# Performance work log

Measured on AMD Instinct MI355X. Metric: run time of the kernel, lower is better.

The kernel has to match this reference:

```python
import jax, jax.numpy as jnp
import numpy as np

N_NODES = 50000
N_EDGES = 640000
IN_FEATS = 512
HID = 128
OUT_FEATS = 128
N_GRAPHS = 256


def setup_inputs() -> dict:
    key = jax.random.key(0)
    ks = jax.random.split(key, 7)
    x = jax.random.normal(ks[0], (N_NODES, IN_FEATS), dtype=jnp.float32)
    edge_index = jax.random.randint(ks[1], (2, N_EDGES), 0, N_NODES, dtype=jnp.int32)
    batch = jnp.sort(jax.random.randint(ks[2], (N_NODES,), 0, N_GRAPHS, dtype=jnp.int32))
    W1 = jax.random.normal(ks[3], (IN_FEATS, HID), dtype=jnp.float32) * (1.0 / np.sqrt(IN_FEATS))
    b1 = jnp.zeros((HID,), jnp.float32)
    W2 = jax.random.normal(ks[4], (HID, OUT_FEATS), dtype=jnp.float32) * (1.0 / np.sqrt(HID))
    b2 = jnp.zeros((OUT_FEATS,), jnp.float32)
    return {"x": x, "W1": W1, "b1": b1, "W2": W2, "b2": b2,
            "edge_index": edge_index, "batch": batch}


def reference(x, W1, b1, W2, b2, edge_index, batch):
    N = x.shape[0]
    loop = jnp.arange(N, dtype=edge_index.dtype)
    # PyG GCNConv default: add self-loops, symmetric deg^-1/2 normalization
    row = jnp.concatenate([edge_index[0], loop])  # source
    col = jnp.concatenate([edge_index[1], loop])  # target
    deg = jax.ops.segment_sum(jnp.ones_like(col, x.dtype), col, num_segments=N)
    dinv = jnp.where(deg > 0, jax.lax.rsqrt(deg), 0.0)
    norm = dinv[row] * dinv[col]  # [E+N]

    def gcn_conv(h, W, b):
        h = h @ W  # linear transform first (PyG order)
        msg = h[row] * norm[:, None]  # gather + scale
        agg = jax.ops.segment_sum(msg, col, num_segments=N)  # scatter-add
        return agg + b

    h = jax.nn.relu(gcn_conv(x, W1, b1))  # dropout is identity in eval mode
    h = gcn_conv(h, W2, b2)
    hs = jax.ops.segment_sum(h, batch, num_segments=N_GRAPHS)  # global_add_pool
    return hs, h
```

## Files before the change

kernel.cpp:

```cpp
#include <hip/hip_runtime.h>
#include <hip/hip_bf16.h>

#define N_NODES  50000
#define N_EDGES  640000
#define IN_FEATS 512
#define HID      128
#define OUT_FEATS 128
#define N_GRAPHS 256

#define SCAN_CHUNK 1024
#define SCAN_BLOCKS ((N_NODES + SCAN_CHUNK - 1) / SCAN_CHUNK)

typedef __attribute__((ext_vector_type(8))) short short8;
typedef __attribute__((ext_vector_type(4))) float f32x4;

__device__ __forceinline__ float bf2f(unsigned u16) {
    return __uint_as_float(u16 << 16);
}
__device__ __forceinline__ unsigned short f2bf(float f) {
    __hip_bfloat16 h = __float2bfloat16(f);
    return *(unsigned short*)&h;
}

__device__ __forceinline__ short8 cvt8(float4 x, float4 y) {
    short8 r;
    r[0] = (short)f2bf(x.x); r[1] = (short)f2bf(x.y);
    r[2] = (short)f2bf(x.z); r[3] = (short)f2bf(x.w);
    r[4] = (short)f2bf(y.x); r[5] = (short)f2bf(y.y);
    r[6] = (short)f2bf(y.z); r[7] = (short)f2bf(y.w);
    return r;
}

__device__ __forceinline__ void gl_lds16(const void* g, void* l) {
    __builtin_amdgcn_global_load_lds(
        (const __attribute__((address_space(1))) void*)g,
        (__attribute__((address_space(3))) void*)l, 16, 0, 0);
}

#define PREP_BLOCKS 644

__global__ __launch_bounds__(256) void k_prep(const float* __restrict__ W1,
                                              const float* __restrict__ W2,
                                              unsigned short* __restrict__ wt1,
                                              unsigned short* __restrict__ wt2,
                                              int* __restrict__ cnt,
                                              float* __restrict__ hs) {
    int b = blockIdx.x;
    int t = threadIdx.x;
    if (b < 196) {
        int i = b * 256 + t;
        if (i < N_NODES) cnt[i] = 0;
    } else if (b < 452) {
        int idx = (b - 196) * 256 + t;
        int n = idx & 127, k = idx >> 7;
        wt1[(size_t)n * IN_FEATS + k] = f2bf(W1[(size_t)k * 128 + n]);
    } else if (b < 516) {
        int idx = (b - 452) * 256 + t;
        int n = idx & 127, k = idx >> 7;
        wt2[(size_t)n * HID + k] = f2bf(W2[(size_t)k * 128 + n]);
    } else {
        int idx = (b - 516) * 256 + t;
        hs[idx] = 0.f;
    }
}


template <int K>
__global__ __launch_bounds__(256, 4) void k_g1c(const float* __restrict__ A,
                                                const unsigned short* __restrict__ Bt,
                                                unsigned short* __restrict__ Cb, int M,
                                                const int* __restrict__ col,
                                                int* __restrict__ cnt, int nblk_gemm) {
    __shared__ float          As[2][2][4][64][4];
    __shared__ unsigned short Bs[2][4][128][8];
    int tid = threadIdx.x;

    if (blockIdx.x >= nblk_gemm) {
        int e4 = ((blockIdx.x - nblk_gemm) * 256 + tid) * 4;
        if (e4 < N_EDGES) {
            int4 c = *(const int4*)(col + e4);
            atomicAdd(&cnt[c.x], 1);
            atomicAdd(&cnt[c.y], 1);
            atomicAdd(&cnt[c.z], 1);
            atomicAdd(&cnt[c.w], 1);
        }
        return;
    }

    int wave = tid >> 6;
    int lane = tid & 63;
    int quad = lane >> 4;
    int l15 = lane & 15;
    int wm = wave >> 1;
    int wn = wave & 1;
    int m0 = blockIdx.x * 64;

#define STAGE(buf, k0) {                                                        \
    _Pragma("unroll")                                                           \
    for (int is = 0; is < 2; ++is) {                                            \
        int c = (wave * 2 + is) * 64 + lane;                                    \
        int h = c >> 8, kq = (c >> 6) & 3, r = c & 63;                          \
        int gr = m0 + r; if (gr >= M) gr = M - 1;                               \
        const float* g = A + (size_t)gr * K + (k0) + kq * 8 + h * 4;            \
        void* l = (char*)&As[buf][0][0][0][0] + (wave * 2 + is) * 1024;         \
        gl_lds16(g, l);                                                         \
    }                                                                           \
    _Pragma("unroll")                                                           \
    for (int is = 0; is < 2; ++is) {                                            \
        int c = (wave * 2 + is) * 64 + lane;                                    \
        int kq = c >> 7, r = c & 127;                                           \
        const unsigned short* g = Bt + (size_t)r * K + (k0) + kq * 8;           \
        void* l = (char*)&Bs[buf][0][0][0] + (wave * 2 + is) * 1024;            \
        gl_lds16(g, l);                                                         \
    }                                                                           \
}

    f32x4 acc[2][4];
#pragma unroll
    for (int i = 0; i < 2; ++i)
#pragma unroll
        for (int j = 0; j < 4; ++j) acc[i][j] = (f32x4){0.f, 0.f, 0.f, 0.f};

    const int NT = K / 32;
    STAGE(0, 0);
    STAGE(1, 32);

#pragma unroll 1
    for (int t = 0; t < NT; ++t) {
        int buf = t & 1;
        if (t == NT - 1) { asm volatile("s_waitcnt vmcnt(0)" ::: "memory"); }
        else             { asm volatile("s_waitcnt vmcnt(4)" ::: "memory"); }
        __builtin_amdgcn_s_barrier();

        float4 lo0 = *(const float4*)&As[buf][0][quad][wm * 32 + l15][0];
        float4 hi0 = *(const float4*)&As[buf][1][quad][wm * 32 + l15][0];
        float4 lo1 = *(const float4*)&As[buf][0][quad][wm * 32 + 16 + l15][0];
        float4 hi1 = *(const float4*)&As[buf][1][quad][wm * 32 + 16 + l15][0];
        short8 bfr[4];
#pragma unroll
        for (int j = 0; j < 4; ++j)
            bfr[j] = *(const short8*)&Bs[buf][quad][wn * 64 + j * 16 + l15][0];

        asm volatile("s_waitcnt lgkmcnt(0)" ::: "memory");
        __builtin_amdgcn_sched_barrier(0);
        __builtin_amdgcn_s_barrier();

        if (t < NT - 2) STAGE(buf, (t + 2) * 32);
        __builtin_amdgcn_sched_barrier(0);

        short8 a0 = cvt8(lo0, hi0);
        short8 a1 = cvt8(lo1, hi1);
#pragma unroll
        for (int j = 0; j < 4; ++j) {
            acc[0][j] = __builtin_amdgcn_mfma_f32_16x16x32_bf16(a0, bfr[j], acc[0][j], 0, 0, 0);
            acc[1][j] = __builtin_amdgcn_mfma_f32_16x16x32_bf16(a1, bfr[j], acc[1][j], 0, 0, 0);
        }
    }
#undef STAGE

#pragma unroll
    for (int i = 0; i < 2; ++i) {
        int rb = m0 + wm * 32 + i * 16 + quad * 4;
#pragma unroll
        for (int j = 0; j < 4; ++j) {
            int colb = wn * 64 + j * 16 + l15;
#pragma unroll
            for (int r2 = 0; r2 < 4; ++r2) {
                int gm = rb + r2;
                if (gm < M) Cb[(size_t)gm * 128 + colb] = f2bf(acc[i][j][r2]);
            }
        }
    }
}


__global__ __launch_bounds__(256) void k_scan_a(const int* __restrict__ cnt,
                                                int* __restrict__ offs,
                                                int* __restrict__ bsum) {
    __shared__ int sums[256];
    int t = threadIdx.x;
    int base = blockIdx.x * SCAN_CHUNK + t * 4;
    int c0 = 0, c1 = 0, c2 = 0, c3 = 0;
    if (base + 3 < N_NODES) {
        int4 v = *(const int4*)(cnt + base);
        c0 = v.x; c1 = v.y; c2 = v.z; c3 = v.w;
    } else {
        if (base + 0 < N_NODES) c0 = cnt[base + 0];
        if (base + 1 < N_NODES) c1 = cnt[base + 1];
        if (base + 2 < N_NODES) c2 = cnt[base + 2];
    }
    int ts = c0 + c1 + c2 + c3;
    sums[t] = ts;
    __syncthreads();
#pragma unroll
    for (int off = 1; off < 256; off <<= 1) {
        int add = (t >= off) ? sums[t - off] : 0;
        __syncthreads();
        sums[t] += add;
        __syncthreads();
    }
    int ex = sums[t] - ts;
    if (base + 3 < N_NODES) {
        int4 o;
        o.x = ex; o.y = ex + c0; o.z = ex + c0 + c1; o.w = ex + c0 + c1 + c2;
        *(int4*)(offs + base) = o;
    } else {
        if (base + 0 < N_NODES) offs[base + 0] = ex;
        if (base + 1 < N_NODES) offs[base + 1] = ex + c0;
        if (base + 2 < N_NODES) offs[base + 2] = ex + c0 + c1;
    }
    if (t == 255) bsum[blockIdx.x] = sums[255];
}

__global__ __launch_bounds__(256) void k_scan_c(const int* __restrict__ cnt,
                                                const int* __restrict__ bsum,
                                                int* __restrict__ offs,
                                                int* __restrict__ cursor,
                                                float* __restrict__ dinv) {
    __shared__ int sb[64];
    int t = threadIdx.x;
    int b = blockIdx.x;
    if (t < 64) sb[t] = (t < SCAN_BLOCKS) ? bsum[t] : 0;
    __syncthreads();
#pragma unroll
    for (int off = 1; off < 64; off <<= 1) {
        int add = 0;
        if (t < 64 && t >= off) add = sb[t - off];
        __syncthreads();
        if (t < 64) sb[t] += add;
        __syncthreads();
    }
    int add = (b == 0) ? 0 : sb[b - 1];
    int base = b * SCAN_CHUNK + t * 4;
    if (base + 3 < N_NODES) {
        int4 o = *(const int4*)(offs + base);
        o.x += add; o.y += add; o.z += add; o.w += add;
        *(int4*)(offs + base) = o;
        *(int4*)(cursor + base) = o;
        int4 c = *(const int4*)(cnt + base);
        float4 d;
        d.x = rsqrtf((float)c.x + 1.0f);
        d.y = rsqrtf((float)c.y + 1.0f);
        d.z = rsqrtf((float)c.z + 1.0f);
        d.w = rsqrtf((float)c.w + 1.0f);
        *(float4*)(dinv + base) = d;
    } else {
#pragma unroll
        for (int j = 0; j < 4; ++j) {
            int i = base + j;
            if (i < N_NODES) {
                int o = offs[i] + add;
                offs[i] = o; cursor[i] = o;
                dinv[i] = rsqrtf((float)cnt[i] + 1.0f);
            }
        }
    }
    if (b == 0 && t == 0) offs[N_NODES] = N_EDGES;
}

__global__ void k_fill(const int* __restrict__ row, const int* __restrict__ col,
                       int* __restrict__ cursor, int* __restrict__ srcIdx) {
    int e4 = (blockIdx.x * blockDim.x + threadIdx.x) * 4;
    if (e4 >= N_EDGES) return;
    int4 r = *(const int4*)(row + e4);
    int4 c = *(const int4*)(col + e4);
    srcIdx[atomicAdd(&cursor[c.x], 1)] = r.x;
    srcIdx[atomicAdd(&cursor[c.y], 1)] = r.y;
    srcIdx[atomicAdd(&cursor[c.z], 1)] = r.z;
    srcIdx[atomicAdd(&cursor[c.w], 1)] = r.w;
}


template <int RELU>
__global__ __launch_bounds__(256) void k_agg(const unsigned* __restrict__ t,
                                             const int* __restrict__ offs,
                                             const int* __restrict__ srcIdx,
                                             const float* __restrict__ dinv,
                                             const float* __restrict__ bias,
                                             unsigned* __restrict__ out_) {
    int wave = threadIdx.x >> 6;
    int lane = threadIdx.x & 63;
    int h = lane >> 5;
    int l = lane & 31;
    int i = blockIdx.x * 4 + wave;
    float di = dinv[i];
    const unsigned* my = t + (size_t)i * 64 + 2 * l;

    float s0 = 0.f, s1 = 0.f, s2 = 0.f, s3 = 0.f;
    {
        uint2 sv = *(const uint2*)my;
        if (h == 0) {
            s0 = bf2f(sv.x & 0xffffu) * di;
            s1 = bf2f(sv.x >> 16) * di;
            s2 = bf2f(sv.y & 0xffffu) * di;
            s3 = bf2f(sv.y >> 16) * di;
        }
    }
    int lo = offs[i], hi = offs[i + 1];
    for (int e = lo; e < hi; e += 16) {
        int idx[8];
        float d[8];
        uint2 v[8];
#pragma unroll
        for (int j = 0; j < 8; ++j) {
            int ee = e + 2 * j + h;
            idx[j] = (ee < hi) ? srcIdx[ee] : i;
        }
#pragma unroll
        for (int j = 0; j < 8; ++j)
            v[j] = *(const uint2*)(t + (size_t)idx[j] * 64 + 2 * l);
#pragma unroll
        for (int j = 0; j < 8; ++j) {
            int ee = e + 2 * j + h;
            d[j] = (ee < hi) ? dinv[idx[j]] : 0.f;
        }
#pragma unroll
        for (int j = 0; j < 8; ++j) {
            s0 = fmaf(bf2f(v[j].x & 0xffffu), d[j], s0);
            s1 = fmaf(bf2f(v[j].x >> 16),     d[j], s1);
            s2 = fmaf(bf2f(v[j].y & 0xffffu), d[j], s2);
            s3 = fmaf(bf2f(v[j].y >> 16),     d[j], s3);
        }
    }
    s0 += __shfl_xor(s0, 32);
    s1 += __shfl_xor(s1, 32);
    s2 += __shfl_xor(s2, 32);
    s3 += __shfl_xor(s3, 32);

    float r0 = s0 * di, r1 = s1 * di, r2 = s2 * di, r3 = s3 * di;
    if (bias) {
        float4 bb = *(const float4*)(bias + 4 * l);
        r0 += bb.x; r1 += bb.y; r2 += bb.z; r3 += bb.w;
    }
    if (RELU) {
        r0 = fmaxf(r0, 0.f); r1 = fmaxf(r1, 0.f);
        r2 = fmaxf(r2, 0.f); r3 = fmaxf(r3, 0.f);
    }
    if (h == 0) {
        uint2 o;
        o.x = (unsigned)f2bf(r0) | ((unsigned)f2bf(r1) << 16);
        o.y = (unsigned)f2bf(r2) | ((unsigned)f2bf(r3) << 16);
        *(uint2*)(out_ + (size_t)i * 64 + 2 * l) = o;
    }
}


__global__ __launch_bounds__(256) void k_gemm2_pool(const unsigned short* __restrict__ G,
                                                    const unsigned short* __restrict__ Bt,
                                                    const float* __restrict__ bias,
                                                    const int* __restrict__ batch,
                                                    float* __restrict__ out,
                                                    float* __restrict__ hs, int M) {
    const int K = HID;
    __shared__ unsigned short As[4][64][8];
    __shared__ unsigned short Bs[4][128][8];
    int tid = threadIdx.x;
    int wave = tid >> 6;
    int lane = tid & 63;
    int quad = lane >> 4;
    int l15 = lane & 15;
    int m0 = blockIdx.x * 64;

    f32x4 acc[8];
#pragma unroll
    for (int nt = 0; nt < 8; ++nt) acc[nt] = (f32x4){0.f, 0.f, 0.f, 0.f};

    int gm_a = m0 + lane; if (gm_a >= M) gm_a = M - 1;
    const unsigned short* ap_base = G + (size_t)gm_a * K + wave * 8;

    for (int k0 = 0; k0 < K; k0 += 32) {
        *(short8*)&As[wave][lane][0] = *(const short8*)(ap_base + k0);
#pragma unroll
        for (int i = 0; i < 2; ++i) {
            int slot = tid + i * 256;
            int bkq = slot >> 7;
            int n = slot & 127;
            *(short8*)&Bs[bkq][n][0] = *(const short8*)(Bt + (size_t)n * K + k0 + bkq * 8);
        }
        __syncthreads();
        short8 a = *(short8*)&As[quad][wave * 16 + l15][0];
#pragma unroll
        for (int nt = 0; nt < 8; ++nt) {
            short8 b = *(short8*)&Bs[quad][nt * 16 + l15][0];
            acc[nt] = __builtin_amdgcn_mfma_f32_16x16x32_bf16(a, b, acc[nt], 0, 0, 0);
        }
        __syncthreads();
    }
    int rb = m0 + wave * 16 + quad * 4;
    int g_[4];
#pragma unroll
    for (int r2 = 0; r2 < 4; ++r2)
        g_[r2] = (rb + r2 < M) ? batch[rb + r2] : -1;
#pragma unroll
    for (int nt = 0; nt < 8; ++nt) {
        int colb = nt * 16 + l15;
        float bcol = bias[colb];
        float v[4];
#pragma unroll
        for (int r2 = 0; r2 < 4; ++r2) {
            v[r2] = acc[nt][r2] + bcol;
            if (rb + r2 < M) out[(size_t)(rb + r2) * 128 + colb] = v[r2];
        }
        float run = v[0];
        int gcur = g_[0];
#pragma unroll
        for (int r2 = 1; r2 < 4; ++r2) {
            if (g_[r2] == gcur) run += v[r2];
            else {
                if (gcur >= 0) atomicAdd(&hs[(size_t)gcur * 128 + colb], run);
                gcur = g_[r2]; run = v[r2];
            }
        }
        if (gcur >= 0) atomicAdd(&hs[(size_t)gcur * 128 + colb], run);
    }
}


extern "C" void kernel_launch(void* const* d_in, const int* in_sizes, int n_in,
                              void* d_out, int out_size, void* d_ws, size_t ws_size,
                              hipStream_t stream) {
    const float* x  = (const float*)d_in[0];
    const float* W1 = (const float*)d_in[1];
    const float* b1 = (const float*)d_in[2];
    const float* W2 = (const float*)d_in[3];
    const float* b2 = (const float*)d_in[4];
    const int*   ei = (const int*)d_in[5];
    const int*   batch = (const int*)d_in[6];
    const int* row = ei;
    const int* col = ei + N_EDGES;

    float* out_hs = (float*)d_out;
    float* out_h  = (float*)d_out + N_GRAPHS * OUT_FEATS;

    char* ws = (char*)d_ws;
    unsigned short* tb   = (unsigned short*)ws;
    unsigned short* h1b  = (unsigned short*)(ws + 12800000);
    unsigned short* gb   = (unsigned short*)(ws + 25600000);
    float* dinv = (float*)(ws + 38400000);
    int*   cnt    = (int*)(ws + 38600000);
    int*   offs   = (int*)(ws + 38800000);
    int*   cursor = (int*)(ws + 39000016);
    int*   srcIdx = (int*)(ws + 39200016);
    int*   bsum   = (int*)(ws + 41761056);
    unsigned short* wt1 = (unsigned short*)(ws + 41761472);
    unsigned short* wt2 = (unsigned short*)(ws + 41892544);

    const int TB = 256;
    const int GB1 = (N_NODES + 63) / 64;
    const int CB  = (N_EDGES / 4 + TB - 1) / TB;

    k_prep<<<PREP_BLOCKS, 256, 0, stream>>>(W1, W2, wt1, wt2, cnt, out_hs);
    k_g1c<IN_FEATS><<<GB1 + CB, 256, 0, stream>>>(x, wt1, tb, N_NODES, col, cnt, GB1);
    k_scan_a<<<SCAN_BLOCKS, 256, 0, stream>>>(cnt, offs, bsum);
    k_scan_c<<<SCAN_BLOCKS, 256, 0, stream>>>(cnt, bsum, offs, cursor, dinv);
    k_fill<<<(N_EDGES / 4 + TB - 1) / TB, TB, 0, stream>>>(row, col, cursor, srcIdx);

    k_agg<1><<<N_NODES / 4, 256, 0, stream>>>((const unsigned*)tb, offs, srcIdx, dinv, b1, (unsigned*)h1b);
    k_agg<0><<<N_NODES / 4, 256, 0, stream>>>((const unsigned*)h1b, offs, srcIdx, dinv, nullptr, (unsigned*)gb);
    k_gemm2_pool<<<(N_NODES + 63) / 64, 256, 0, stream>>>(gb, wt2, b2, batch, out_h, out_hs, N_NODES);
}
```

Before: 329.8 us.

## Double K-tile depth in first GEMM and use XOR-swizzled LDS layout

Raises the K tile of the layer-1 GEMM from 32 to 64, halving the number of barrier-separated iterations and doubling the in-flight async global-to-LDS loads per stage. The shared-memory layout changes to row-major tiles with an XOR swizzle on 16-byte columns, intended to avoid bank conflicts on the fragment reads. LDS use doubles and launch bounds drop to 2 blocks per SM, which may reduce occupancy and latency hiding.

Result: faster. 321.3 us (-2.6%).

```diff
diff --git a/kernel.cpp b/kernel.cpp
--- a/kernel.cpp
+++ b/kernel.cpp
@@ -66,13 +66,13 @@
 
 
 template <int K>
-__global__ __launch_bounds__(256, 4) void k_g1c(const float* __restrict__ A,
+__global__ __launch_bounds__(256, 2) void k_g1c(const float* __restrict__ A,
                                                 const unsigned short* __restrict__ Bt,
                                                 unsigned short* __restrict__ Cb, int M,
                                                 const int* __restrict__ col,
                                                 int* __restrict__ cnt, int nblk_gemm) {
-    __shared__ float          As[2][2][4][64][4];
-    __shared__ unsigned short Bs[2][4][128][8];
+    __shared__ float          As[2][64][64];
+    __shared__ unsigned short Bs[2][128][64];
     int tid = threadIdx.x;
 
     if (blockIdx.x >= nblk_gemm) {
@@ -97,20 +97,24 @@
 
 #define STAGE(buf, k0) {                                                        \
     _Pragma("unroll")                                                           \
-    for (int is = 0; is < 2; ++is) {                                            \
-        int c = (wave * 2 + is) * 64 + lane;                                    \
-        int h = c >> 8, kq = (c >> 6) & 3, r = c & 63;                          \
+    for (int is = 0; is < 4; ++is) {                                            \
+        int a_ = wave * 4 + is;                             \
+        int c = a_ * 64 + lane;                              \
+        int r = c >> 4, pcol = c & 15;                                          \
+        int lcol = pcol ^ (r & 7);                                              \
         int gr = m0 + r; if (gr >= M) gr = M - 1;                               \
-        const float* g = A + (size_t)gr * K + (k0) + kq * 8 + h * 4;            \
-        void* l = (char*)&As[buf][0][0][0][0] + (wave * 2 + is) * 1024;         \
+        const float* g = A + (size_t)gr * K + (k0) + lcol * 4;                  \
+        void* l = (char*)&As[buf][0][0] + a_ * 1024;                            \
         gl_lds16(g, l);                                                         \
     }                                                                           \
     _Pragma("unroll")                                                           \
-    for (int is = 0; is < 2; ++is) {                                            \
-        int c = (wave * 2 + is) * 64 + lane;                                    \
-        int kq = c >> 7, r = c & 127;                                           \
-        const unsigned short* g = Bt + (size_t)r * K + (k0) + kq * 8;           \
-        void* l = (char*)&Bs[buf][0][0][0] + (wave * 2 + is) * 1024;            \
+    for (int is = 0; is < 4; ++is) {                                            \
+        int a_ = wave * 4 + is;                                                 \
+        int c = a_ * 64 + lane;                                                 \
+        int r = c >> 3, pcol = c & 7;                                           \
+        int lcol = pcol ^ (r & 7);                                              \
+        const unsigned short* g = Bt + (size_t)r * K + (k0) + lcol * 8;         \
+        void* l = (char*)&Bs[buf][0][0] + a_ * 1024;                            \
         gl_lds16(g, l);                                                         \
     }                                                                           \
 }
@@ -121,39 +125,57 @@
 #pragma unroll
         for (int j = 0; j < 4; ++j) acc[i][j] = (f32x4){0.f, 0.f, 0.f, 0.f};
 
-    const int NT = K / 32;
+    const int NT = K / 64;
     STAGE(0, 0);
-    STAGE(1, 32);
+    STAGE(1, 64);
 
 #pragma unroll 1
     for (int t = 0; t < NT; ++t) {
         int buf = t & 1;
         if (t == NT - 1) { asm volatile("s_waitcnt vmcnt(0)" ::: "memory"); }
-        else             { asm volatile("s_waitcnt vmcnt(4)" ::: "memory"); }
+        else             { asm volatile("s_waitcnt vmcnt(8)" ::: "memory"); }
         __builtin_amdgcn_s_barrier();
 
-        float4 lo0 = *(const float4*)&As[buf][0][quad][wm * 32 + l15][0];
-        float4 hi0 = *(const float4*)&As[buf][1][quad][wm * 32 + l15][0];
-        float4 lo1 = *(const float4*)&As[buf][0][quad][wm * 32 + 16 + l15][0];
-        float4 hi1 = *(const float4*)&As[buf][1][quad][wm * 32 + 16 + l15][0];
-        short8 bfr[4];
-#pragma unroll
-        for (int j = 0; j < 4; ++j)
-            bfr[j] = *(const short8*)&Bs[buf][quad][wn * 64 + j * 16 + l15][0];
+        const char* abase = (const char*)&As[buf][0][0];
+        const char* bbase = (const char*)&Bs[buf][0][0];
+        float4 ax[2][2], ay[2][2];
+#pragma unroll
+        for (int kh = 0; kh < 2; ++kh)
+#pragma unroll
+            for (int i = 0; i < 2; ++i) {
+                int r = wm * 32 + i * 16 + l15;
+                int lc = kh * 8 + quad * 2;
+                int p0 = lc ^ (r & 7);
+                ax[kh][i] = *(const float4*)(abase + r * 256 + p0 * 16);
+                ay[kh][i] = *(const float4*)(abase + r * 256 + (p0 ^ 1) * 16);
+            }
+        short8 bfr[2][4];
+#pragma unroll
+        for (int kh = 0; kh < 2; ++kh)
+#pragma unroll
+            for (int j = 0; j < 4; ++j) {
+                int r = wn * 64 + j * 16 + l15;
+                int lc = kh * 4 + quad;
+                int p = lc ^ (r & 7);
+                bfr[kh][j] = *(const short8*)(bbase + r * 128 + p * 16);
+            }
 
         asm volatile("s_waitcnt lgkmcnt(0)" ::: "memory");
         __builtin_amdgcn_sched_barrier(0);
         __builtin_amdgcn_s_barrier();
 
-        if (t < NT - 2) STAGE(buf, (t + 2) * 32);
+        if (t < NT - 2) STAGE(buf, (t + 2) * 64);
         __builtin_amdgcn_sched_barrier(0);
 
-        short8 a0 = cvt8(lo0, hi0);
-        short8 a1 = cvt8(lo1, hi1);
-#pragma unroll
-        for (int j = 0; j < 4; ++j) {
-            acc[0][j] = __builtin_amdgcn_mfma_f32_16x16x32_bf16(a0, bfr[j], acc[0][j], 0, 0, 0);
-            acc[1][j] = __builtin_amdgcn_mfma_f32_16x16x32_bf16(a1, bfr[j], acc[1][j], 0, 0, 0);
+#pragma unroll
+        for (int kh = 0; kh < 2; ++kh) {
+            short8 a0 = cvt8(ax[kh][0], ay[kh][0]);
+            short8 a1 = cvt8(ax[kh][1], ay[kh][1]);
+#pragma unroll
+            for (int j = 0; j < 4; ++j) {
+                acc[0][j] = __builtin_amdgcn_mfma_f32_16x16x32_bf16(a0, bfr[kh][j], acc[0][j], 0, 0, 0);
+                acc[1][j] = __builtin_amdgcn_mfma_f32_16x16x32_bf16(a1, bfr[kh][j], acc[1][j], 0, 0, 0);
+            }
         }
     }
 #undef STAGE
```
